# Performance work log

Hardware: AMD Instinct MI355X
Metric: run time of the kernel (lower is better)

## Reference

```python
import jax, jax.numpy as jnp
import numpy as np

TEMPERATURE = 16.0  # sqrt(d_k) for d_k=256

def setup_inputs() -> dict:
    key = jax.random.key(0)
    q = jax.random.normal(key, (32, 1024, 256), dtype=jnp.float32)
    return {"q": q}

def reference(q):
    # attn = q @ q^T  (b, l, l)
    attn = jnp.einsum('bld,bmd->blm', q, q)
    # data-dependent zero mask -> -inf fill (before temperature scaling, matching torch order)
    zero_mask = attn == 0.0
    attn = jnp.where(zero_mask, -jnp.inf, attn / TEMPERATURE)
    attn = jax.nn.softmax(attn, axis=2)
    # rows that were fully -inf produce NaN -> zero them out
    attn = jnp.where(jnp.isnan(attn), 0.0, attn)
    # dropout is identity in eval/reference mode
    output = jnp.einsum('blm,bmd->bld', attn, q)
    return (output, attn)
```

## Files before the change

### kernel.cpp

```cpp
#include <hip/hip_runtime.h>
#include <stdint.h>

#define NB 32
#define NL 1024
#define ND 256

typedef __attribute__((ext_vector_type(8))) __bf16 bf16x8;
typedef __attribute__((ext_vector_type(4))) uint16_t u16x4;
typedef __attribute__((ext_vector_type(4))) float f32x4;

__device__ __forceinline__ uint16_t f2bf(float f) {
  union { float f; uint32_t u; } v; v.f = f;
  return (uint16_t)((v.u + 0x7fffu + ((v.u >> 16) & 1u)) >> 16);
}
__device__ __forceinline__ float bf2f(uint16_t h) {
  union { uint32_t u; float f; } v; v.u = ((uint32_t)h) << 16;
  return v.f;
}

#define GLD_LDS16(g, l)                                                        \
  __builtin_amdgcn_global_load_lds(                                            \
      (__attribute__((address_space(1))) void*)(g),                            \
      (__attribute__((address_space(3))) void*)(l), 16, 0, 0)

__global__ __launch_bounds__(256) void convert_kernel(
    const float* __restrict__ q, uint16_t* __restrict__ qb,
    uint16_t* __restrict__ qt) {
  __shared__ uint16_t tile[64][72];
  int b = blockIdx.z;
  int l0 = blockIdx.x * 64, d0 = blockIdx.y * 64;
  int t = threadIdx.x;
  int r = t >> 4;
  int c4 = (t & 15) * 4;
  const float* qsrc = q + (size_t)b * NL * ND;
  uint16_t* qbb = qb + (size_t)b * NL * ND;
  uint16_t* qtb = qt + (size_t)b * ND * NL;
#pragma unroll
  for (int i = 0; i < 4; i++) {
    int row = r + 16 * i;
    float4 v = *(const float4*)(qsrc + (size_t)(l0 + row) * ND + d0 + c4);
    ushort4 h;
    h.x = f2bf(v.x); h.y = f2bf(v.y); h.z = f2bf(v.z); h.w = f2bf(v.w);
    *(ushort4*)(qbb + (size_t)(l0 + row) * ND + d0 + c4) = h;
    tile[row][c4 + 0] = h.x; tile[row][c4 + 1] = h.y;
    tile[row][c4 + 2] = h.z; tile[row][c4 + 3] = h.w;
  }
  __syncthreads();
#pragma unroll
  for (int i = 0; i < 4; i++) {
    int drow = r + 16 * i;
    ushort4 h;
    h.x = tile[c4 + 0][drow]; h.y = tile[c4 + 1][drow];
    h.z = tile[c4 + 2][drow]; h.w = tile[c4 + 3][drow];
    *(ushort4*)(qtb + (size_t)(d0 + drow) * NL + l0 + c4) = h;
  }
}

__global__ __launch_bounds__(512) void attn_kernel(
    const uint16_t* __restrict__ qb, const uint16_t* __restrict__ qt,
    float* __restrict__ attn, float* __restrict__ out) {
  __shared__ alignas(16) uint16_t P[64 * 1024];
  __shared__ alignas(16) uint16_t pool[8192];
  int b = blockIdx.z;
  int m0 = blockIdx.x * 64;
  const uint16_t* Q = qb + (size_t)b * NL * ND;
  const uint16_t* Bt = qt + (size_t)b * ND * NL;
  int tid = threadIdx.x, lane = tid & 63, wave = tid >> 6;
  int wmw = wave >> 1;
  int wnh = wave & 1;
  int quad = lane >> 4, l15 = lane & 15;
  int mw = wmw * 16 + l15;

  bf16x8 af[8];
#pragma unroll
  for (int kk = 0; kk < 8; kk++)
    af[kk] = *(const bf16x8*)(Q + (size_t)(m0 + mw) * ND + kk * 32 + quad * 8);

  {
    int row = tid >> 2, cc = tid & 3;
    int sw = (row >> 1) & 3;
    GLD_LDS16(Q + (size_t)row * ND + ((cc ^ sw) * 8),
              pool + (size_t)(wave * 64) * 8);
  }
  float rsum[4] = {0.f, 0.f, 0.f, 0.f};
  const float kf = 0.09016844005555f;
  int buf = 0;
  for (int ns = 0; ns < 8; ns++) {
    f32x4 sacc[4] = {};
    int n0 = ns * 128;
#pragma unroll
    for (int kk = 0; kk < 8; kk++) {
      __syncthreads();
      int step = ns * 8 + kk + 1;
      if (step < 64) {
        int nn0 = (step >> 3) * 128, kk0 = (step & 7) * 32;
        int row = tid >> 2, cc = tid & 3;
        int sw = (row >> 1) & 3;
        GLD_LDS16(Q + (size_t)(nn0 + row) * ND + kk0 + ((cc ^ sw) * 8),
                  pool + (size_t)((buf ^ 1) * 512 + wave * 64) * 8);
      }
      const uint16_t* Bb = pool + buf * 4096;
      bf16x8 bq[4];
#pragma unroll
      for (int t = 0; t < 4; t++) {
        int rb = wnh * 64 + t * 16 + l15;
        bq[t] = *(const bf16x8*)(Bb + rb * 32 + ((quad ^ ((rb >> 1) & 3)) * 8));
      }
#pragma unroll
      for (int t = 0; t < 4; t++)
        sacc[t] = __builtin_amdgcn_mfma_f32_16x16x32_bf16(af[kk], bq[t],
                                                          sacc[t], 0, 0, 0);
      buf ^= 1;
    }
#pragma unroll
    for (int t = 0; t < 4; t++) {
      int n = n0 + wnh * 64 + t * 16 + l15;
      int g = n >> 3, e = n & 7;
#pragma unroll
      for (int j = 0; j < 4; j++) {
        int m = wmw * 16 + quad * 4 + j;
        float s = sacc[t][j];
        float ev = (s == 0.0f) ? 0.0f : __builtin_amdgcn_exp2f(s * kf);
        P[m * 1024 + (((g ^ (m & 7)) << 3) + e)] = f2bf(ev);
        rsum[j] += ev;
      }
    }
  }

  __syncthreads();
  float* poolf = (float*)pool;
#pragma unroll
  for (int j = 0; j < 4; j++) {
    float v = rsum[j];
    v += __shfl_xor(v, 1, 64);
    v += __shfl_xor(v, 2, 64);
    v += __shfl_xor(v, 4, 64);
    v += __shfl_xor(v, 8, 64);
    if (l15 == 0) poolf[(wmw * 16 + quad * 4 + j) * 2 + wnh] = v;
  }
  __syncthreads();
  float invo[4];
#pragma unroll
  for (int j = 0; j < 4; j++) {
    int r = wmw * 16 + quad * 4 + j;
    float s = poolf[r * 2] + poolf[r * 2 + 1];
    invo[j] = (s > 0.f) ? 1.f / s : 0.f;
  }
  int xm = tid >> 3, xs = tid & 7;
  float sx = poolf[xm * 2] + poolf[xm * 2 + 1];
  float invx = (sx > 0.f) ? 1.f / sx : 0.f;
  __syncthreads();

  f32x4 pacc[8] = {};
  {
#pragma unroll
    for (int i = 0; i < 2; i++) {
      int c = i * 512 + tid;
      int row = c >> 2, cc = c & 3;
      int sw = (row >> 1) & 3;
      GLD_LDS16(Bt + (size_t)row * NL + ((cc ^ sw) * 8),
                pool + (size_t)(i * 512 + wave * 64) * 8);
    }
  }
  float* attnb = attn + ((size_t)b * NL + m0) * NL;
  for (int c = 0; c < 32; c++) {
    __syncthreads();
    int gx = c * 4 + (xs >> 1);
    u16x4 h =
        *(const u16x4*)(P + xm * 1024 + (((gx ^ (xm & 7)) << 3) + (xs & 1) * 4));
    float4 v4;
    v4.x = bf2f(h[0]) * invx; v4.y = bf2f(h[1]) * invx;
    v4.z = bf2f(h[2]) * invx; v4.w = bf2f(h[3]) * invx;
    *(float4*)(attnb + (size_t)xm * NL + c * 32 + xs * 4) = v4;
    int gP = c * 4 + quad;
    bf16x8 pa = *(const bf16x8*)(P + mw * 1024 + ((gP ^ (mw & 7)) << 3));
    bf16x8 vb[8];
#pragma unroll
    for (int t = 0; t < 8; t++) {
      int rb = wnh * 128 + t * 16 + l15;
      vb[t] = *(const bf16x8*)(pool + rb * 32 + ((quad ^ ((rb >> 1) & 3)) * 8));
    }
    __syncthreads();
    if (c < 31) {
      int n0c = (c + 1) * 32;
#pragma unroll
      for (int i = 0; i < 2; i++) {
        int cc2 = i * 512 + tid;
        int row = cc2 >> 2, ccc = cc2 & 3;
        int sw = (row >> 1) & 3;
        GLD_LDS16(Bt + (size_t)row * NL + n0c + ((ccc ^ sw) * 8),
                  pool + (size_t)(i * 512 + wave * 64) * 8);
      }
    }
#pragma unroll
    for (int t = 0; t < 8; t++)
      pacc[t] = __builtin_amdgcn_mfma_f32_16x16x32_bf16(pa, vb[t], pacc[t],
                                                        0, 0, 0);
  }

  float* O = out + (size_t)b * NL * ND + (size_t)m0 * ND;
#pragma unroll
  for (int t = 0; t < 8; t++) {
    int col = wnh * 128 + t * 16 + l15;
#pragma unroll
    for (int j = 0; j < 4; j++) {
      int r = wmw * 16 + quad * 4 + j;
      O[(size_t)r * ND + col] = pacc[t][j] * invo[j];
    }
  }
}

extern "C" void kernel_launch(void* const* d_in, const int* in_sizes, int n_in,
                              void* d_out, int out_size, void* d_ws,
                              size_t ws_size, hipStream_t stream) {
  (void)in_sizes; (void)n_in; (void)out_size; (void)ws_size;
  const float* q = (const float*)d_in[0];
  float* out = (float*)d_out;
  float* attn = out + (size_t)NB * NL * ND;
  uint16_t* qb = (uint16_t*)d_ws;
  uint16_t* qt = qb + (size_t)NB * NL * ND;

  convert_kernel<<<dim3(16, 4, NB), 256, 0, stream>>>(q, qb, qt);
  attn_kernel<<<dim3(16, 1, NB), 512, 0, stream>>>(qb, qt, attn, out);
}
```

Measured before the change: 263.0 us.

## Load B operands directly from global into registers, dropping LDS staging and barriers

Both GEMM phases now have each wave load its B fragments (Q rows and the transposed Q) straight from global memory into registers, double-buffered in registers. This replaces the shared LDS pool filled by global_load_lds and removes the per-step __syncthreads barriers. The goal is less barrier overhead and LDS traffic. The cost is that the two waves sharing a column half (and, in phase 1, all 16 blocks of a batch) fetch the same B tiles separately, so global/L2 traffic and register use go up.

```diff
diff --git a/kernel.cpp b/kernel.cpp
--- a/kernel.cpp
+++ b/kernel.cpp
@@ -17,11 +17,6 @@
   union { uint32_t u; float f; } v; v.u = ((uint32_t)h) << 16;
   return v.f;
 }
-
-#define GLD_LDS16(g, l)                                                        \
-  __builtin_amdgcn_global_load_lds(                                            \
-      (__attribute__((address_space(1))) void*)(g),                            \
-      (__attribute__((address_space(3))) void*)(l), 16, 0, 0)
 
 __global__ __launch_bounds__(256) void convert_kernel(
     const float* __restrict__ q, uint16_t* __restrict__ qb,
@@ -60,7 +55,7 @@
     const uint16_t* __restrict__ qb, const uint16_t* __restrict__ qt,
     float* __restrict__ attn, float* __restrict__ out) {
   __shared__ alignas(16) uint16_t P[64 * 1024];
-  __shared__ alignas(16) uint16_t pool[8192];
+  __shared__ float rsums[64][2];
   int b = blockIdx.z;
   int m0 = blockIdx.x * 64;
   const uint16_t* Q = qb + (size_t)b * NL * ND;
@@ -76,41 +71,30 @@
   for (int kk = 0; kk < 8; kk++)
     af[kk] = *(const bf16x8*)(Q + (size_t)(m0 + mw) * ND + kk * 32 + quad * 8);
 
-  {
-    int row = tid >> 2, cc = tid & 3;
-    int sw = (row >> 1) & 3;
-    GLD_LDS16(Q + (size_t)row * ND + ((cc ^ sw) * 8),
-              pool + (size_t)(wave * 64) * 8);
-  }
   float rsum[4] = {0.f, 0.f, 0.f, 0.f};
   const float kf = 0.09016844005555f;
-  int buf = 0;
+  int nrow = wnh * 64 + l15;
   for (int ns = 0; ns < 8; ns++) {
+    int n0 = ns * 128;
     f32x4 sacc[4] = {};
-    int n0 = ns * 128;
+    bf16x8 bq[2][4];
+#pragma unroll
+    for (int t = 0; t < 4; t++)
+      bq[0][t] = *(const bf16x8*)(Q + (size_t)(n0 + nrow + t * 16) * ND +
+                                  quad * 8);
 #pragma unroll
     for (int kk = 0; kk < 8; kk++) {
-      __syncthreads();
-      int step = ns * 8 + kk + 1;
-      if (step < 64) {
-        int nn0 = (step >> 3) * 128, kk0 = (step & 7) * 32;
-        int row = tid >> 2, cc = tid & 3;
-        int sw = (row >> 1) & 3;
-        GLD_LDS16(Q + (size_t)(nn0 + row) * ND + kk0 + ((cc ^ sw) * 8),
-                  pool + (size_t)((buf ^ 1) * 512 + wave * 64) * 8);
-      }
-      const uint16_t* Bb = pool + buf * 4096;
-      bf16x8 bq[4];
+      if (kk < 7) {
 #pragma unroll
-      for (int t = 0; t < 4; t++) {
-        int rb = wnh * 64 + t * 16 + l15;
-        bq[t] = *(const bf16x8*)(Bb + rb * 32 + ((quad ^ ((rb >> 1) & 3)) * 8));
+        for (int t = 0; t < 4; t++)
+          bq[(kk + 1) & 1][t] =
+              *(const bf16x8*)(Q + (size_t)(n0 + nrow + t * 16) * ND +
+                               (kk + 1) * 32 + quad * 8);
       }
 #pragma unroll
       for (int t = 0; t < 4; t++)
-        sacc[t] = __builtin_amdgcn_mfma_f32_16x16x32_bf16(af[kk], bq[t],
-                                                          sacc[t], 0, 0, 0);
-      buf ^= 1;
+        sacc[t] = __builtin_amdgcn_mfma_f32_16x16x32_bf16(
+            af[kk], bq[kk & 1][t], sacc[t], 0, 0, 0);
     }
 #pragma unroll
     for (int t = 0; t < 4; t++) {
@@ -127,8 +111,6 @@
     }
   }
 
-  __syncthreads();
-  float* poolf = (float*)pool;
 #pragma unroll
   for (int j = 0; j < 4; j++) {
     float v = rsum[j];
@@ -136,66 +118,52 @@
     v += __shfl_xor(v, 2, 64);
     v += __shfl_xor(v, 4, 64);
     v += __shfl_xor(v, 8, 64);
-    if (l15 == 0) poolf[(wmw * 16 + quad * 4 + j) * 2 + wnh] = v;
+    if (l15 == 0) rsums[wmw * 16 + quad * 4 + j][wnh] = v;
   }
   __syncthreads();
   float invo[4];
 #pragma unroll
   for (int j = 0; j < 4; j++) {
     int r = wmw * 16 + quad * 4 + j;
-    float s = poolf[r * 2] + poolf[r * 2 + 1];
+    float s = rsums[r][0] + rsums[r][1];
     invo[j] = (s > 0.f) ? 1.f / s : 0.f;
   }
   int xm = tid >> 3, xs = tid & 7;
-  float sx = poolf[xm * 2] + poolf[xm * 2 + 1];
+  float sx = rsums[xm][0] + rsums[xm][1];
   float invx = (sx > 0.f) ? 1.f / sx : 0.f;
-  __syncthreads();
 
   f32x4 pacc[8] = {};
-  {
+  bf16x8 vb[2][8], pa[2];
+  int drow = wnh * 128 + l15;
 #pragma unroll
-    for (int i = 0; i < 2; i++) {
-      int c = i * 512 + tid;
-      int row = c >> 2, cc = c & 3;
-      int sw = (row >> 1) & 3;
-      GLD_LDS16(Bt + (size_t)row * NL + ((cc ^ sw) * 8),
-                pool + (size_t)(i * 512 + wave * 64) * 8);
+  for (int t = 0; t < 8; t++)
+    vb[0][t] = *(const bf16x8*)(Bt + (size_t)(drow + t * 16) * NL + quad * 8);
+  pa[0] = *(const bf16x8*)(P + mw * 1024 + ((quad ^ (mw & 7)) << 3));
+  float* attnb = attn + ((size_t)b * NL + m0) * NL;
+#pragma unroll 2
+  for (int c = 0; c < 32; c++) {
+    int cur = c & 1;
+    if (c < 31) {
+#pragma unroll
+      for (int t = 0; t < 8; t++)
+        vb[cur ^ 1][t] = *(const bf16x8*)(Bt + (size_t)(drow + t * 16) * NL +
+                                          (c + 1) * 32 + quad * 8);
+      int gP = (c + 1) * 4 + quad;
+      pa[cur ^ 1] = *(const bf16x8*)(P + mw * 1024 + ((gP ^ (mw & 7)) << 3));
     }
-  }
-  float* attnb = attn + ((size_t)b * NL + m0) * NL;
-  for (int c = 0; c < 32; c++) {
-    __syncthreads();
-    int gx = c * 4 + (xs >> 1);
-    u16x4 h =
-        *(const u16x4*)(P + xm * 1024 + (((gx ^ (xm & 7)) << 3) + (xs & 1) * 4));
-    float4 v4;
-    v4.x = bf2f(h[0]) * invx; v4.y = bf2f(h[1]) * invx;
-    v4.z = bf2f(h[2]) * invx; v4.w = bf2f(h[3]) * invx;
-    *(float4*)(attnb + (size_t)xm * NL + c * 32 + xs * 4) = v4;
-    int gP = c * 4 + quad;
-    bf16x8 pa = *(const bf16x8*)(P + mw * 1024 + ((gP ^ (mw & 7)) << 3));
-    bf16x8 vb[8];
-#pragma unroll
-    for (int t = 0; t < 8; t++) {
-      int rb = wnh * 128 + t * 16 + l15;
-      vb[t] = *(const bf16x8*)(pool + rb * 32 + ((quad ^ ((rb >> 1) & 3)) * 8));
-    }
-    __syncthreads();
-    if (c < 31) {
-      int n0c = (c + 1) * 32;
-#pragma unroll
-      for (int i = 0; i < 2; i++) {
-        int cc2 = i * 512 + tid;
-        int row = cc2 >> 2, ccc = cc2 & 3;
-        int sw = (row >> 1) & 3;
-        GLD_LDS16(Bt + (size_t)row * NL + n0c + ((ccc ^ sw) * 8),
-                  pool + (size_t)(i * 512 + wave * 64) * 8);
-      }
+    {
+      int gx = c * 4 + (xs >> 1);
+      u16x4 h = *(const u16x4*)(P + xm * 1024 +
+                                (((gx ^ (xm & 7)) << 3) + (xs & 1) * 4));
+      float4 v4;
+      v4.x = bf2f(h[0]) * invx; v4.y = bf2f(h[1]) * invx;
+      v4.z = bf2f(h[2]) * invx; v4.w = bf2f(h[3]) * invx;
+      *(float4*)(attnb + (size_t)xm * NL + c * 32 + xs * 4) = v4;
     }
 #pragma unroll
     for (int t = 0; t < 8; t++)
-      pacc[t] = __builtin_amdgcn_mfma_f32_16x16x32_bf16(pa, vb[t], pacc[t],
-                                                        0, 0, 0);
+      pacc[t] = __builtin_amdgcn_mfma_f32_16x16x32_bf16(pa[cur], vb[cur][t],
+                                                        pacc[t], 0, 0, 0);
   }
 
   float* O = out + (size_t)b * NL * ND + (size_t)m0 * ND;
```

Result: slower. 402.2 us (+53.0%).
